# Performance work log

Measured on AMD Instinct MI355X. Metric: run time of the kernel, lower is better.

## Reference

```python
import jax, jax.numpy as jnp
import numpy as np

N_NODES = 10000
N_EDGES = 160000
C = 128           # channel multiplicity
D_DOWN = 64       # node_feats_down '64x0e'
D_RAD = 8         # radial basis size
AVG_NEIGH = 16.0
INV_SQRT3 = 1.0 / np.sqrt(3.0)  # CG coeff for 1o x 1o -> 0e


def setup_inputs() -> dict:
    key = jax.random.key(0)
    ks = jax.random.split(key, 20)
    inp = {
        "node_attrs": jax.random.normal(ks[0], (N_NODES, 10), jnp.float32),
        "node_feats": jax.random.normal(ks[1], (N_NODES, 4 * C), jnp.float32),
        "edge_attrs": jax.random.normal(ks[2], (N_EDGES, 4), jnp.float32),
        "edge_feats": jax.random.uniform(ks[3], (N_EDGES, D_RAD), jnp.float32),
        "edge_index": jax.random.randint(ks[4], (N_EDGES, 2), 0, N_NODES, jnp.int32),
        # linear_up: 128x0e+128x1o -> 128x0e+128x1o (per-irrep channel mixing)
        "W_up0": jax.random.normal(ks[5], (C, C), jnp.float32),
        "W_up1": jax.random.normal(ks[6], (C, C), jnp.float32),
        # linear_down: 128x0e+128x1o -> 64x0e (only scalars map)
        "W_down": jax.random.normal(ks[7], (C, D_DOWN), jnp.float32),
        # radial MLP [136, 256, 256, 256, 512]
        "Wm0": jax.random.normal(ks[8], (D_RAD + 2 * D_DOWN, 256), jnp.float32),
        "Wm1": jax.random.normal(ks[9], (256, 256), jnp.float32),
        "Wm2": jax.random.normal(ks[10], (256, 256), jnp.float32),
        "Wm3": jax.random.normal(ks[11], (256, 4 * C), jnp.float32),
        # linear: irreps_mid (2x128x0e + 2x128x1o) -> 128x0e+128x1o
        "W_lin0": jax.random.normal(ks[12], (2 * C, C), jnp.float32),
        "W_lin1": jax.random.normal(ks[13], (2 * C, C), jnp.float32),
        # skip_linear: 128x0e+128x1o -> 128x0e+128x1o
        "W_skip0": jax.random.normal(ks[14], (C, C), jnp.float32),
        "W_skip1": jax.random.normal(ks[15], (C, C), jnp.float32),
    }
    return inp


def _split(x):
    # [N, 512] -> scalars [N,128], vectors [N,128,3]
    return x[:, :C], x[:, C:].reshape(-1, C, 3)


def _irrep_linear(s, v, W0, W1):
    # e3nn Linear with 1/sqrt(fan_in) normalization, per-irrep
    a = (s @ W0) / np.sqrt(C)
    b = jnp.einsum("nic,ij->njc", v, W1) / np.sqrt(C)
    return a, b


def reference(node_attrs, node_feats, edge_attrs, edge_feats, edge_index,
              W_up0, W_up1, W_down, Wm0, Wm1, Wm2, Wm3,
              W_lin0, W_lin1, W_skip0, W_skip1):
    n_nodes = node_feats.shape[0]
    sender = edge_index[:, 0]
    receiver = edge_index[:, 1]

    s, v = _split(node_feats)

    # skip connection
    sc_s, sc_v = _irrep_linear(s, v, W_skip0, W_skip1)
    sc = jnp.concatenate([sc_s, sc_v.reshape(n_nodes, 3 * C)], axis=-1)

    # linear_up / linear_down
    up_s, up_v = _irrep_linear(s, v, W_up0, W_up1)
    down = (s @ W_down) / np.sqrt(C)  # [N, 64]

    # radial MLP on augmented edge feats
    aug = jnp.concatenate([edge_feats, down[sender], down[receiver]], axis=-1)  # [E,136]
    h = jax.nn.silu((aug @ Wm0) / np.sqrt(aug.shape[-1]))
    h = jax.nn.silu((h @ Wm1) / np.sqrt(256.0))
    h = jax.nn.silu((h @ Wm2) / np.sqrt(256.0))
    tpw = (h @ Wm3) / np.sqrt(256.0)  # [E, 512]
    w1, w2, w3, w4 = tpw[:, :C], tpw[:, C:2*C], tpw[:, 2*C:3*C], tpw[:, 3*C:]

    # per-edge CG tensor product (uvu, external weights)
    xs = up_s[sender]           # [E,128] gathered 0e
    xv = up_v[sender]           # [E,128,3] gathered 1o
    y0 = edge_attrs[:, :1]      # [E,1]   sh 0e
    yv = edge_attrs[:, 1:4]     # [E,3]   sh 1o

    out0a = w1 * xs * y0                                       # 0e x 0e -> 0e
    out0b = w4 * jnp.einsum("eic,ec->ei", xv, yv) * INV_SQRT3  # 1o x 1o -> 0e
    out1a = (w2 * xs)[:, :, None] * yv[:, None, :]             # 0e x 1o -> 1o
    out1b = w3[:, :, None] * xv * y0[:, :, None]               # 1o x 0e -> 1o

    mid0 = jnp.concatenate([out0a, out0b], axis=-1)  # [E,256]
    mid1 = jnp.concatenate([out1a, out1b], axis=1)   # [E,256,3]

    # scatter-sum messages to receivers
    m0 = jax.ops.segment_sum(mid0, receiver, num_segments=n_nodes)
    m1 = jax.ops.segment_sum(mid1, receiver, num_segments=n_nodes)

    # final per-irrep linear, divided by avg_num_neighbors
    msg_s = (m0 @ W_lin0) / np.sqrt(2.0 * C) / AVG_NEIGH                       # [N,128]
    msg_v = jnp.einsum("nic,ij->njc", m1, W_lin1) / np.sqrt(2.0 * C) / AVG_NEIGH  # [N,128,3]

    # reshape_irreps: [N, channels, 1+3]
    out = jnp.concatenate([msg_s[:, :, None], msg_v], axis=-1)  # [N,128,4]
    return out, sc
```

## Files before the change

### kernel.cpp

```cpp
#include <hip/hip_runtime.h>
#include <cmath>

#define NN 10000
#define NE 160000
#define INV_SQRT_C 0.08838834764831845f
#define INV_SQRT3F 0.5773502691896258f

typedef _Float16 f16x8 __attribute__((ext_vector_type(8)));
typedef _Float16 f16x4 __attribute__((ext_vector_type(4)));
typedef _Float16 f16x2 __attribute__((ext_vector_type(2)));
typedef float    f32x4 __attribute__((ext_vector_type(4)));

__device__ __forceinline__ float silu_f(float x) {
  return x / (1.f + __expf(-x));
}

__device__ __forceinline__ void wconv_one(
    int bx, const float* __restrict__ src, _Float16* __restrict__ dst,
    int Korig, int Kpad, int N, float scale, int P) {
  int total = Kpad * N;
  for (int t = bx * 256 + threadIdx.x; t < total; t += 128 * 256) {
    int n = t % N;
    int k = t / N;
    int kb = k >> 5, kk = k & 31;
    int sub = n & (P - 1);
    int n_l = (n & ~(P - 1)) | ((sub & 15) * (P >> 4) + (sub >> 4));
    float v = (k < Korig) ? src[(size_t)k * N + n_l] * scale : 0.f;
    dst[((size_t)(kb * N + n) << 5) + kk] = (_Float16)v;
  }
}

__global__ __launch_bounds__(256) void prep(
    const float* __restrict__ s0, const float* __restrict__ s1,
    const float* __restrict__ s2, const float* __restrict__ s3,
    const float* __restrict__ s4, const float* __restrict__ s5,
    _Float16* __restrict__ d0, _Float16* __restrict__ d1,
    _Float16* __restrict__ d2, _Float16* __restrict__ d3,
    _Float16* __restrict__ d4, _Float16* __restrict__ d5,
    const float* __restrict__ feats,
    const float* __restrict__ W_up0, const float* __restrict__ W_skip0,
    const float* __restrict__ W_down,
    const float* __restrict__ W_up1, const float* __restrict__ W_skip1,
    _Float16* __restrict__ UPH, _Float16* __restrict__ DOWNH,
    float* __restrict__ out_sc,
    const int* __restrict__ edge_index,
    int* __restrict__ CNT, int* __restrict__ CNT2) {
  __shared__ float ls[16 * 512];
  const int b = blockIdx.x;
  const int t = threadIdx.x;

  if (b < 768) {
    const int job = b >> 7, bx = b & 127;
    switch (job) {
      case 0: wconv_one(bx, s0, d0, 136, 160, 256, 0.08574929257125442f, 64); break;
      case 1: wconv_one(bx, s1, d1, 256, 256, 256, 0.0625f, 64); break;
      case 2: wconv_one(bx, s2, d2, 256, 256, 256, 0.0625f, 64); break;
      case 3: wconv_one(bx, s3, d3, 256, 256, 512, 0.0625f, 32); break;
      case 4: wconv_one(bx, s4, d4, 256, 256, 128, 1.0f / 256.0f, 32); break;
      default: wconv_one(bx, s5, d5, 256, 256, 128, 1.0f / 256.0f, 32); break;
    }
    return;
  }
  if (b >= 2018) {
    int e = (b - 2018) * 256 + t;
    if (e < NE) {
      int2 sr = *(const int2*)&edge_index[(size_t)e * 2];
      atomicAdd(&CNT[sr.y], 1);
      atomicAdd(&CNT2[sr.x], 1);
    }
    return;
  }

  const int nb = b - 768;
  if (nb < 625) {
    const int n0 = nb * 16;
    for (int f = t; f < 16 * 128; f += 256) {
      int r = f >> 7, c = f & 127;
      ls[r * 128 + c] = feats[(size_t)(n0 + r) * 512 + c];
    }
    __syncthreads();
    {
      int j = t & 127, g = t >> 7;
      float au[8] = {0, 0, 0, 0, 0, 0, 0, 0};
      float ak[8] = {0, 0, 0, 0, 0, 0, 0, 0};
      for (int i = 0; i < 128; ++i) {
        float wu = W_up0[(size_t)i * 128 + j];
        float wk = W_skip0[(size_t)i * 128 + j];
#pragma unroll
        for (int r = 0; r < 8; ++r) {
          float s = ls[(g * 8 + r) * 128 + i];
          au[r] += s * wu;
          ak[r] += s * wk;
        }
      }
#pragma unroll
      for (int r = 0; r < 8; ++r) {
        int n = n0 + g * 8 + r;
        UPH[(size_t)n * 512 + j] = (_Float16)(au[r] * INV_SQRT_C);
        out_sc[(size_t)n * 512 + j] = ak[r] * INV_SQRT_C;
      }
    }
    {
      int j = t & 63, g = t >> 6;
      float ad[4] = {0, 0, 0, 0};
      for (int i = 0; i < 128; ++i) {
        float wd = W_down[(size_t)i * 64 + j];
#pragma unroll
        for (int r = 0; r < 4; ++r) ad[r] += ls[(g * 4 + r) * 128 + i] * wd;
      }
#pragma unroll
      for (int r = 0; r < 4; ++r)
        DOWNH[(size_t)(n0 + g * 4 + r) * 64 + j] = (_Float16)(ad[r] * INV_SQRT_C);
    }
  } else {
    const int n0 = (nb - 625) * 16;
    for (int f = t; f < 16 * 384; f += 256) {
      int r = f / 384, c = f % 384;
      int i = c / 3, cc = c - i * 3;
      ls[(r * 128 + i) * 4 + cc] = feats[(size_t)(n0 + r) * 512 + 128 + c];
    }
    __syncthreads();
    const float4* lv = (const float4*)ls;
    int j = t & 127, g = t >> 7;
    float au[8][3], ak[8][3];
#pragma unroll
    for (int r = 0; r < 8; ++r)
#pragma unroll
      for (int c = 0; c < 3; ++c) { au[r][c] = 0.f; ak[r][c] = 0.f; }
    for (int i = 0; i < 128; ++i) {
      float wu = W_up1[(size_t)i * 128 + j];
      float wk = W_skip1[(size_t)i * 128 + j];
#pragma unroll
      for (int r = 0; r < 8; ++r) {
        float4 v = lv[(g * 8 + r) * 128 + i];
        au[r][0] += v.x * wu; au[r][1] += v.y * wu; au[r][2] += v.z * wu;
        ak[r][0] += v.x * wk; ak[r][1] += v.y * wk; ak[r][2] += v.z * wk;
      }
    }
#pragma unroll
    for (int r = 0; r < 8; ++r) {
      int n = n0 + g * 8 + r;
#pragma unroll
      for (int c = 0; c < 3; ++c) {
        UPH[(size_t)n * 512 + 128 + j * 3 + c] = (_Float16)(au[r][c] * INV_SQRT_C);
        out_sc[(size_t)n * 512 + 128 + j * 3 + c] = ak[r][c] * INV_SQRT_C;
      }
    }
  }
}

__device__ __forceinline__ void scan_one(const int* __restrict__ CNT,
                                         int* __restrict__ OFF,
                                         int* __restrict__ CUR, int* ts) {
  const int t = threadIdx.x;
  const int base = t * 10;
  int loc[10];
  int s = 0;
#pragma unroll
  for (int i = 0; i < 10; ++i) {
    int idx = base + i;
    int v = (idx < NN) ? CNT[idx] : 0;
    loc[i] = s;
    s += v;
  }
  ts[t] = s;
  __syncthreads();
  for (int off = 1; off < 1024; off <<= 1) {
    int v = (t >= off) ? ts[t - off] : 0;
    __syncthreads();
    ts[t] += v;
    __syncthreads();
  }
  int tp = (t > 0) ? ts[t - 1] : 0;
#pragma unroll
  for (int i = 0; i < 10; ++i) {
    int idx = base + i;
    if (idx < NN) {
      OFF[idx] = tp + loc[i];
      CUR[idx] = tp + loc[i];
    }
  }
  if (t == 1023) OFF[NN] = ts[1023];
}

__global__ __launch_bounds__(1024) void k_scan2(
    const int* __restrict__ CNT, int* __restrict__ OFF, int* __restrict__ CUR,
    const int* __restrict__ CNT2, int* __restrict__ OFF2, int* __restrict__ CUR2) {
  __shared__ int ts[1024];
  if (blockIdx.x == 0) scan_one(CNT, OFF, CUR, ts);
  else                 scan_one(CNT2, OFF2, CUR2, ts);
}

__global__ void k_fill2(const int* __restrict__ edge_index,
                        int* __restrict__ CUR, int* __restrict__ EIDX,
                        int* __restrict__ CUR2, int* __restrict__ SIDX) {
  int e = blockIdx.x * blockDim.x + threadIdx.x;
  if (e < NE) {
    int2 sr = *(const int2*)&edge_index[(size_t)e * 2];
    int ps = atomicAdd(&CUR2[sr.x], 1);
    SIDX[ps] = e;
    int pr = atomicAdd(&CUR[sr.y], 1);
    EIDX[pr] = ps;
  }
}

__device__ __forceinline__ void mlp_layer_256(
    const _Float16* In, _Float16* Out, const _Float16* __restrict__ Wz,
    int m, int g, int wv) {
  f32x4 acc[4][4];
  f32x4 zero4 = {0.f, 0.f, 0.f, 0.f};
#pragma unroll
  for (int rt = 0; rt < 4; ++rt)
#pragma unroll
    for (int ct = 0; ct < 4; ++ct) acc[rt][ct] = zero4;

#pragma unroll
  for (int kb = 0; kb < 8; ++kb) {
    f16x8 a[4], b[4];
#pragma unroll
    for (int rt = 0; rt < 4; ++rt) {
      int row = rt * 16 + m;
      a[rt] = *(const f16x8*)&In[row * 256 + (((kb * 2 + (g >> 1)) ^ m) << 4) + (g & 1) * 8];
    }
#pragma unroll
    for (int ct = 0; ct < 4; ++ct)
      b[ct] = *(const f16x8*)&Wz[((size_t)(kb * 256 + wv * 64 + ct * 16 + m) << 5) + g * 8];
#pragma unroll
    for (int rt = 0; rt < 4; ++rt)
#pragma unroll
      for (int ct = 0; ct < 4; ++ct)
        acc[rt][ct] = __builtin_amdgcn_mfma_f32_16x16x32_f16(a[rt], b[ct], acc[rt][ct], 0, 0, 0);
  }
#pragma unroll
  for (int rt = 0; rt < 4; ++rt)
#pragma unroll
    for (int q = 0; q < 4; ++q) {
      int row = rt * 16 + g * 4 + q;
      f16x4 pk;
#pragma unroll
      for (int ct = 0; ct < 4; ++ct) pk[ct] = (_Float16)silu_f(acc[rt][ct][q]);
      int blk = (wv * 4 + (m >> 2)) ^ (row & 15);
      *(f16x4*)&Out[row * 256 + (blk << 4) + (m & 3) * 4] = pk;
    }
}

__global__ __launch_bounds__(256, 2) void edge_mlp(
    const float* __restrict__ edge_attrs,
    const float* __restrict__ edge_feats,
    const int* __restrict__ edge_index,
    const int* __restrict__ SIDX,
    const _Float16* __restrict__ DOWNH,
    const _Float16* __restrict__ UPH,
    const _Float16* __restrict__ W0h, const _Float16* __restrict__ W1h,
    const _Float16* __restrict__ W2h, const _Float16* __restrict__ W3h,
    const _Float16* __restrict__ WL0h, const _Float16* __restrict__ WL1h,
    _Float16* __restrict__ MIDs) {
  __shared__ _Float16 HA[64 * 256];
  __shared__ _Float16 HB[64 * 256];

  const int tid = threadIdx.x;
  const int lane = tid & 63;
  const int wv = tid >> 6;
  const int m = lane & 15;
  const int g = lane >> 4;
  const int e0 = blockIdx.x * 64;
  const int nw = wv * 64;

  int el_r[4], snd_r[4], rcv_r[4];
#pragma unroll
  for (int rt = 0; rt < 4; ++rt) {
    el_r[rt] = SIDX[e0 + rt * 16 + m];
    int2 sr = *(const int2*)&edge_index[(size_t)el_r[rt] * 2];
    snd_r[rt] = sr.x;
    rcv_r[rt] = sr.y;
  }

  f32x4 zero4 = {0.f, 0.f, 0.f, 0.f};
  f16x8 zf = {0, 0, 0, 0, 0, 0, 0, 0};

  {
    f32x4 acc[4][4];
#pragma unroll
    for (int rt = 0; rt < 4; ++rt)
#pragma unroll
      for (int ct = 0; ct < 4; ++ct) acc[rt][ct] = zero4;

#pragma unroll
    for (int kb = 0; kb < 5; ++kb) {
      const int k0 = kb * 32 + g * 8;
      f16x8 a[4], b[4];
#pragma unroll
      for (int rt = 0; rt < 4; ++rt) {
        if (k0 == 0) {
          const float* ef = &edge_feats[(size_t)el_r[rt] * 8];
          float4 f0 = *(const float4*)ef;
          float4 f1 = *(const float4*)(ef + 4);
          f16x8 av;
          av[0] = (_Float16)f0.x; av[1] = (_Float16)f0.y;
          av[2] = (_Float16)f0.z; av[3] = (_Float16)f0.w;
          av[4] = (_Float16)f1.x; av[5] = (_Float16)f1.y;
          av[6] = (_Float16)f1.z; av[7] = (_Float16)f1.w;
          a[rt] = av;
        } else if (k0 < 72) {
          a[rt] = *(const f16x8*)&DOWNH[(size_t)snd_r[rt] * 64 + (k0 - 8)];
        } else if (k0 < 136) {
          a[rt] = *(const f16x8*)&DOWNH[(size_t)rcv_r[rt] * 64 + (k0 - 72)];
        } else {
          a[rt] = zf;
        }
      }
#pragma unroll
      for (int ct = 0; ct < 4; ++ct)
        b[ct] = *(const f16x8*)&W0h[((size_t)(kb * 256 + nw + ct * 16 + m) << 5) + g * 8];
#pragma unroll
      for (int rt = 0; rt < 4; ++rt)
#pragma unroll
        for (int ct = 0; ct < 4; ++ct)
          acc[rt][ct] = __builtin_amdgcn_mfma_f32_16x16x32_f16(a[rt], b[ct], acc[rt][ct], 0, 0, 0);
    }
#pragma unroll
    for (int rt = 0; rt < 4; ++rt)
#pragma unroll
      for (int q = 0; q < 4; ++q) {
        int row = rt * 16 + g * 4 + q;
        f16x4 pk;
#pragma unroll
        for (int ct = 0; ct < 4; ++ct) pk[ct] = (_Float16)silu_f(acc[rt][ct][q]);
        int blk = (wv * 4 + (m >> 2)) ^ (row & 15);
        *(f16x4*)&HA[row * 256 + (blk << 4) + (m & 3) * 4] = pk;
      }
  }
  __syncthreads();

  mlp_layer_256(HA, HB, W1h, m, g, wv);
  __syncthreads();
  mlp_layer_256(HB, HA, W2h, m, g, wv);
  __syncthreads();

  _Float16* SW = HB;
  _Float16* SP = HB + 64 * 128;

  const int e_loc = lane;
  const int ers = (e_loc ^ (e_loc >> 3)) & 7;
  const int elc = SIDX[e0 + e_loc];
  const int snd_e = edge_index[(size_t)elc * 2];
  const _Float16* uprow = &UPH[(size_t)snd_e * 512];

  auto qgemm = [&](int qbase, f32x4 (&accq)[4][2]) {
#pragma unroll
    for (int rt = 0; rt < 4; ++rt)
#pragma unroll
      for (int ct = 0; ct < 2; ++ct) accq[rt][ct] = zero4;
#pragma unroll
    for (int kb = 0; kb < 8; ++kb) {
      f16x8 a[4], b[2];
#pragma unroll
      for (int rt = 0; rt < 4; ++rt) {
        int row = rt * 16 + m;
        a[rt] = *(const f16x8*)&HA[row * 256 + (((kb * 2 + (g >> 1)) ^ m) << 4) + (g & 1) * 8];
      }
#pragma unroll
      for (int ct = 0; ct < 2; ++ct)
        b[ct] = *(const f16x8*)&W3h[((size_t)(kb * 512 + qbase + wv * 32 + ct * 16 + m) << 5) + g * 8];
#pragma unroll
      for (int rt = 0; rt < 4; ++rt)
#pragma unroll
        for (int ct = 0; ct < 2; ++ct)
          accq[rt][ct] = __builtin_amdgcn_mfma_f32_16x16x32_f16(a[rt], b[ct], accq[rt][ct], 0, 0, 0);
    }
  };

  auto sw_write = [&](const f32x4 (&accq)[4][2]) {
#pragma unroll
    for (int rt = 0; rt < 4; ++rt)
#pragma unroll
      for (int r4 = 0; r4 < 4; ++r4) {
        int row = rt * 16 + g * 4 + r4;
        int rs = (row ^ (row >> 3)) & 7;
        f16x2 pk;
        pk[0] = (_Float16)accq[rt][0][r4];
        pk[1] = (_Float16)accq[rt][1][r4];
        int blk = ((wv * 2 + (m >> 3)) ^ rs) & 7;
        *(f16x2*)&SW[row * 128 + (blk << 4) + (m & 7) * 2] = pk;
      }
  };

  auto fold = [&](const _Float16* __restrict__ WLh, int qpart, f32x4 (&P)[4][2]) {
#pragma unroll
    for (int rt = 0; rt < 4; ++rt)
#pragma unroll
      for (int ct = 0; ct < 2; ++ct) P[rt][ct] = zero4;
#pragma unroll
    for (int kb = 0; kb < 4; ++kb) {
      f16x8 a[4], b[2];
#pragma unroll
      for (int rt = 0; rt < 4; ++rt) {
        int row = rt * 16 + m;
        int rs = (row ^ (row >> 3)) & 7;
        a[rt] = *(const f16x8*)&SP[row * 128 + ((((kb * 2 + (g >> 1)) ^ rs) & 7) << 4) + (g & 1) * 8];
      }
#pragma unroll
      for (int ct = 0; ct < 2; ++ct)
        b[ct] = *(const f16x8*)&WLh[((size_t)((qpart * 4 + kb) * 128 + wv * 32 + ct * 16 + m) << 5) + g * 8];
#pragma unroll
      for (int rt = 0; rt < 4; ++rt)
#pragma unroll
        for (int ct = 0; ct < 2; ++ct)
          P[rt][ct] = __builtin_amdgcn_mfma_f32_16x16x32_f16(a[rt], b[ct], P[rt][ct], 0, 0, 0);
    }
  };

  auto tp_xs = [&]() {
#pragma unroll
    for (int cch = 0; cch < 4; ++cch) {
      int ib = nw / 2 + cch * 8;
      int blk = ((ib >> 4) ^ ers) & 7;
      int off = e_loc * 128 + (blk << 4) + (ib & 15);
      f16x8 swv = *(const f16x8*)&SW[off];
      f16x8 upv = *(const f16x8*)&uprow[ib];
      f16x8 pr = swv * upv;
      *(f16x8*)&SP[off] = pr;
    }
  };

  _Float16 xvb[96];
  auto load_xv = [&]() {
#pragma unroll
    for (int u = 0; u < 12; ++u) {
      f16x8 t = *(const f16x8*)&uprow[128 + wv * 96 + u * 8];
#pragma unroll
      for (int z = 0; z < 8; ++z) xvb[u * 8 + z] = t[z];
    }
  };

  auto tp_w4 = [&]() {
    float4 ea = *(const float4*)&edge_attrs[(size_t)elc * 4];
#pragma unroll
    for (int cch = 0; cch < 4; ++cch) {
      int ib = nw / 2 + cch * 8;
      int blk = ((ib >> 4) ^ ers) & 7;
      int off = e_loc * 128 + (blk << 4) + (ib & 15);
      f16x8 swv = *(const f16x8*)&SW[off];
      f16x8 outv;
#pragma unroll
      for (int z = 0; z < 8; ++z) {
        int k = cch * 8 + z;
        float d = (float)xvb[k * 3] * ea.y + (float)xvb[k * 3 + 1] * ea.z +
                  (float)xvb[k * 3 + 2] * ea.w;
        outv[z] = (_Float16)((float)swv[z] * d);
      }
      *(f16x8*)&SP[off] = outv;
    }
  };

  auto tp_w3 = [&](int c) {
#pragma unroll
    for (int cch = 0; cch < 4; ++cch) {
      int ib = nw / 2 + cch * 8;
      int blk = ((ib >> 4) ^ ers) & 7;
      int off = e_loc * 128 + (blk << 4) + (ib & 15);
      f16x8 swv = *(const f16x8*)&SW[off];
      f16x8 outv;
#pragma unroll
      for (int z = 0; z < 8; ++z) {
        int k = cch * 8 + z;
        outv[z] = swv[z] * xvb[k * 3 + c];
      }
      *(f16x8*)&SP[off] = outv;
    }
  };

  f32x4 accqA[4][2], accqB[4][2];
  f32x4 P1[4][2], P4[4][2], P2[4][2], P3[4][2];

  qgemm(0, accqA);
  sw_write(accqA);
  tp_xs();
  qgemm(384, accqB);
  __syncthreads();
  fold(WL0h, 0, P1);
  sw_write(accqB);
  load_xv();
  __syncthreads();
  tp_w4();
  qgemm(128, accqA);
  __syncthreads();
  fold(WL0h, 1, P4);
  sw_write(accqA);

#pragma unroll
  for (int rt = 0; rt < 4; ++rt)
#pragma unroll
    for (int r4 = 0; r4 < 4; ++r4) {
      int row = rt * 16 + g * 4 + r4;
      int elw = SIDX[e0 + row];
      float4 ea = *(const float4*)&edge_attrs[(size_t)elw * 4];
      f16x2 pk;
      pk[0] = (_Float16)(ea.x * P1[rt][0][r4] + INV_SQRT3F * P4[rt][0][r4]);
      pk[1] = (_Float16)(ea.x * P1[rt][1][r4] + INV_SQRT3F * P4[rt][1][r4]);
      *(f16x2*)&MIDs[(size_t)(e0 + row) * 512 + wv * 32 + m * 2] = pk;
    }
  __syncthreads();
  tp_xs();
  qgemm(256, accqB);
  __syncthreads();
  fold(WL1h, 0, P2);
  sw_write(accqB);
  __syncthreads();

#pragma unroll
  for (int c = 0; c < 3; ++c) {
    tp_w3(c);
    __syncthreads();
    fold(WL1h, 1, P3);
#pragma unroll
    for (int rt = 0; rt < 4; ++rt)
#pragma unroll
      for (int r4 = 0; r4 < 4; ++r4) {
        int row = rt * 16 + g * 4 + r4;
        int elw = SIDX[e0 + row];
        float4 ea = *(const float4*)&edge_attrs[(size_t)elw * 4];
        float yvc = (c == 0) ? ea.y : (c == 1) ? ea.z : ea.w;
        f16x2 pk;
        pk[0] = (_Float16)(yvc * P2[rt][0][r4] + ea.x * P3[rt][0][r4]);
        pk[1] = (_Float16)(yvc * P2[rt][1][r4] + ea.x * P3[rt][1][r4]);
        *(f16x2*)&MIDs[(size_t)(e0 + row) * 512 + 128 + c * 128 + wv * 32 + m * 2] = pk;
      }
    if (c < 2) __syncthreads();
  }
}

__global__ __launch_bounds__(256) void gather_msg(
    const _Float16* __restrict__ MIDs, const int* __restrict__ OFF,
    const int* __restrict__ EIDX, float* __restrict__ out) {
  __shared__ int eb[256];
  __shared__ float os[512];
  const int n = blockIdx.x;
  const int t = threadIdx.x;
  const int beg = OFF[n], end = OFF[n + 1];
  float a0 = 0.f, a1 = 0.f;
  for (int base = beg; base < end; base += 256) {
    int cnt = min(256, end - base);
    __syncthreads();
    if (t < cnt) eb[t] = EIDX[base + t];
    __syncthreads();
    int k = 0;
    for (; k + 4 <= cnt; k += 4) {
      int e0_ = eb[k], e1_ = eb[k + 1], e2_ = eb[k + 2], e3_ = eb[k + 3];
      f16x2 v0 = *(const f16x2*)&MIDs[(size_t)e0_ * 512 + t * 2];
      f16x2 v1 = *(const f16x2*)&MIDs[(size_t)e1_ * 512 + t * 2];
      f16x2 v2 = *(const f16x2*)&MIDs[(size_t)e2_ * 512 + t * 2];
      f16x2 v3 = *(const f16x2*)&MIDs[(size_t)e3_ * 512 + t * 2];
      a0 += (float)v0[0] + (float)v1[0] + (float)v2[0] + (float)v3[0];
      a1 += (float)v0[1] + (float)v1[1] + (float)v2[1] + (float)v3[1];
    }
    for (; k < cnt; ++k) {
      f16x2 v = *(const f16x2*)&MIDs[(size_t)eb[k] * 512 + t * 2];
      a0 += (float)v[0];
      a1 += (float)v[1];
    }
  }
#pragma unroll
  for (int u = 0; u < 2; ++u) {
    int x = t * 2 + u;
    float a = u ? a1 : a0;
    int dst;
    if (x < 128) {
      dst = x * 4;
    } else {
      int xm = x - 128;
      int c = xm >> 7, j = xm & 127;
      dst = j * 4 + 1 + c;
    }
    os[dst] = a;
  }
  __syncthreads();
  *(float2*)&out[(size_t)n * 512 + t * 2] = *(const float2*)&os[t * 2];
}

extern "C" void kernel_launch(void* const* d_in, const int* in_sizes, int n_in,
                              void* d_out, int out_size, void* d_ws, size_t ws_size,
                              hipStream_t stream) {
  const float* node_feats = (const float*)d_in[1];
  const float* edge_attrs = (const float*)d_in[2];
  const float* edge_feats = (const float*)d_in[3];
  const int*   edge_index = (const int*)d_in[4];
  const float* W_up0   = (const float*)d_in[5];
  const float* W_up1   = (const float*)d_in[6];
  const float* W_down  = (const float*)d_in[7];
  const float* Wm0     = (const float*)d_in[8];
  const float* Wm1     = (const float*)d_in[9];
  const float* Wm2     = (const float*)d_in[10];
  const float* Wm3     = (const float*)d_in[11];
  const float* W_lin0  = (const float*)d_in[12];
  const float* W_lin1  = (const float*)d_in[13];
  const float* W_skip0 = (const float*)d_in[14];
  const float* W_skip1 = (const float*)d_in[15];
  float* out = (float*)d_out;

  char* ws = (char*)d_ws;
  size_t off = 0;
  auto alloc = [&](size_t bytes) {
    void* p = ws + off;
    off = (off + bytes + 255) & ~(size_t)255;
    return p;
  };
  _Float16* UPH   = (_Float16*)alloc((size_t)NN * 512 * 2);
  _Float16* DOWNH = (_Float16*)alloc((size_t)NN * 64 * 2);
  _Float16* W0h   = (_Float16*)alloc(160 * 256 * 2);
  _Float16* W1h   = (_Float16*)alloc(256 * 256 * 2);
  _Float16* W2h   = (_Float16*)alloc(256 * 256 * 2);
  _Float16* W3h   = (_Float16*)alloc(256 * 512 * 2);
  _Float16* WL0h  = (_Float16*)alloc(256 * 128 * 2);
  _Float16* WL1h  = (_Float16*)alloc(256 * 128 * 2);
  int*      CNTS  = (int*)alloc((size_t)2 * NN * 4);
  int*      CNT   = CNTS;
  int*      CNT2  = CNTS + NN;
  int*      OFF   = (int*)alloc((size_t)(NN + 1) * 4);
  int*      CUR   = (int*)alloc((size_t)NN * 4);
  int*      EIDX  = (int*)alloc((size_t)NE * 4);
  int*      OFF2  = (int*)alloc((size_t)(NN + 1) * 4);
  int*      CUR2  = (int*)alloc((size_t)NN * 4);
  int*      SIDX  = (int*)alloc((size_t)NE * 4);
  _Float16* MIDs  = (_Float16*)alloc((size_t)NE * 512 * 2);

  hipMemsetAsync(CNTS, 0, (size_t)2 * NN * 4, stream);

  prep<<<2643, 256, 0, stream>>>(Wm0, Wm1, Wm2, Wm3, W_lin0, W_lin1,
                                 W0h, W1h, W2h, W3h, WL0h, WL1h,
                                 node_feats, W_up0, W_skip0, W_down,
                                 W_up1, W_skip1,
                                 UPH, DOWNH, out + (size_t)NN * 512,
                                 edge_index, CNT, CNT2);

  k_scan2<<<2, 1024, 0, stream>>>(CNT, OFF, CUR, CNT2, OFF2, CUR2);
  k_fill2<<<625, 256, 0, stream>>>(edge_index, CUR, EIDX, CUR2, SIDX);

  edge_mlp<<<2500, 256, 0, stream>>>(edge_attrs, edge_feats, edge_index, SIDX,
                                     DOWNH, UPH, W0h, W1h, W2h, W3h, WL0h, WL1h,
                                     MIDs);
  gather_msg<<<NN, 256, 0, stream>>>(MIDs, OFF, EIDX, out);
}
```

Before: 461.5 us.

## Move node up/skip/down linears to MFMA fp16 GEMM kernel

Splits the old prep kernel into a weight-conversion/edge-count kernel and a new prep2 kernel. prep2 computes the up, skip and down node linears with fp16 MFMA tiles from swizzled shared memory instead of scalar fp32 FMA loops. Up and skip weights are packed into one fp16 buffer so both outputs share the A tiles. It adds an extra kernel launch and computes the fp32 skip output from fp16-rounded inputs, which costs accuracy.

```diff
diff --git a/kernel.cpp b/kernel.cpp
--- a/kernel.cpp
+++ b/kernel.cpp
@@ -30,25 +30,46 @@
   }
 }
 
-__global__ __launch_bounds__(256) void prep(
+__device__ __forceinline__ void wconv_pair(
+    int bx, const float* __restrict__ A, const float* __restrict__ B,
+    _Float16* __restrict__ dst, float scale) {
+  int tgl = bx * 256 + threadIdx.x;
+  int n = tgl & 255;
+  int k = tgl >> 8;
+  int kb = k >> 5, kk = k & 31;
+  int sub = n & 63;
+  int n_l = (n & ~63) | ((sub & 15) * 4 + (sub >> 4));
+  float v = ((n_l < 128) ? A[(size_t)k * 128 + n_l]
+                         : B[(size_t)k * 128 + (n_l - 128)]) * scale;
+  dst[((size_t)(kb * 256 + n) << 5) + kk] = (_Float16)v;
+}
+
+__device__ __forceinline__ void wconv_dn(
+    int bx, const float* __restrict__ src, _Float16* __restrict__ dst,
+    float scale) {
+  int tgl = bx * 256 + threadIdx.x;
+  int n = tgl & 63;
+  int k = tgl >> 6;
+  int kb = k >> 5, kk = k & 31;
+  float v = src[(size_t)k * 64 + n] * scale;
+  dst[((size_t)(kb * 64 + n) << 5) + kk] = (_Float16)v;
+}
+
+__global__ __launch_bounds__(256) void wconv9(
     const float* __restrict__ s0, const float* __restrict__ s1,
     const float* __restrict__ s2, const float* __restrict__ s3,
     const float* __restrict__ s4, const float* __restrict__ s5,
     _Float16* __restrict__ d0, _Float16* __restrict__ d1,
     _Float16* __restrict__ d2, _Float16* __restrict__ d3,
     _Float16* __restrict__ d4, _Float16* __restrict__ d5,
-    const float* __restrict__ feats,
     const float* __restrict__ W_up0, const float* __restrict__ W_skip0,
+    const float* __restrict__ W_up1, const float* __restrict__ W_skip1,
     const float* __restrict__ W_down,
-    const float* __restrict__ W_up1, const float* __restrict__ W_skip1,
-    _Float16* __restrict__ UPH, _Float16* __restrict__ DOWNH,
-    float* __restrict__ out_sc,
+    _Float16* __restrict__ WS0h, _Float16* __restrict__ WS1h,
+    _Float16* __restrict__ WDh,
     const int* __restrict__ edge_index,
     int* __restrict__ CNT, int* __restrict__ CNT2) {
-  __shared__ float ls[16 * 512];
   const int b = blockIdx.x;
-  const int t = threadIdx.x;
-
   if (b < 768) {
     const int job = b >> 7, bx = b & 127;
     switch (job) {
@@ -59,93 +80,167 @@
       case 4: wconv_one(bx, s4, d4, 256, 256, 128, 1.0f / 256.0f, 32); break;
       default: wconv_one(bx, s5, d5, 256, 256, 128, 1.0f / 256.0f, 32); break;
     }
-    return;
-  }
-  if (b >= 2018) {
-    int e = (b - 2018) * 256 + t;
+  } else if (b < 896) {
+    wconv_pair(b - 768, W_up0, W_skip0, WS0h, INV_SQRT_C);
+  } else if (b < 1024) {
+    wconv_pair(b - 896, W_up1, W_skip1, WS1h, INV_SQRT_C);
+  } else if (b < 1056) {
+    wconv_dn(b - 1024, W_down, WDh, INV_SQRT_C);
+  } else {
+    int e = (b - 1056) * 256 + threadIdx.x;
     if (e < NE) {
       int2 sr = *(const int2*)&edge_index[(size_t)e * 2];
       atomicAdd(&CNT[sr.y], 1);
       atomicAdd(&CNT2[sr.x], 1);
     }
-    return;
-  }
-
-  const int nb = b - 768;
-  if (nb < 625) {
-    const int n0 = nb * 16;
-    for (int f = t; f < 16 * 128; f += 256) {
-      int r = f >> 7, c = f & 127;
-      ls[r * 128 + c] = feats[(size_t)(n0 + r) * 512 + c];
+  }
+}
+
+__global__ __launch_bounds__(256) void prep2(
+    const float* __restrict__ feats,
+    const _Float16* __restrict__ WS0h, const _Float16* __restrict__ WS1h,
+    const _Float16* __restrict__ WDh,
+    _Float16* __restrict__ UPH, _Float16* __restrict__ DOWNH,
+    float* __restrict__ out_sc) {
+  __shared__ _Float16 As[64 * 128];
+  const int b = blockIdx.x;
+  const int t = threadIdx.x;
+  const int lane = t & 63;
+  const int wv = t >> 6;
+  const int m = lane & 15;
+  const int g = lane >> 4;
+  f32x4 zero4 = {0.f, 0.f, 0.f, 0.f};
+  f16x8 zf = {0, 0, 0, 0, 0, 0, 0, 0};
+
+  if (b < 157) {
+    const int n0 = b * 64;
+    for (int idx = t; idx < 1024; idx += 256) {
+      int r = idx >> 4, c8 = idx & 15;
+      int n = n0 + r;
+      f16x8 av = zf;
+      if (n < NN) {
+        const float* src = &feats[(size_t)n * 512 + c8 * 8];
+        float4 f0 = *(const float4*)src;
+        float4 f1 = *(const float4*)(src + 4);
+        av[0] = (_Float16)f0.x; av[1] = (_Float16)f0.y;
+        av[2] = (_Float16)f0.z; av[3] = (_Float16)f0.w;
+        av[4] = (_Float16)f1.x; av[5] = (_Float16)f1.y;
+        av[6] = (_Float16)f1.z; av[7] = (_Float16)f1.w;
+      }
+      int sb = (c8 >> 1) ^ (r & 7);
+      *(f16x8*)&As[r * 128 + (sb << 4) + (c8 & 1) * 8] = av;
     }
     __syncthreads();
-    {
-      int j = t & 127, g = t >> 7;
-      float au[8] = {0, 0, 0, 0, 0, 0, 0, 0};
-      float ak[8] = {0, 0, 0, 0, 0, 0, 0, 0};
-      for (int i = 0; i < 128; ++i) {
-        float wu = W_up0[(size_t)i * 128 + j];
-        float wk = W_skip0[(size_t)i * 128 + j];
-#pragma unroll
-        for (int r = 0; r < 8; ++r) {
-          float s = ls[(g * 8 + r) * 128 + i];
-          au[r] += s * wu;
-          ak[r] += s * wk;
+
+    f32x4 acc[4][4];
+    f32x4 acc2[4];
+#pragma unroll
+    for (int rt = 0; rt < 4; ++rt) {
+      acc2[rt] = zero4;
+#pragma unroll
+      for (int ct = 0; ct < 4; ++ct) acc[rt][ct] = zero4;
+    }
+#pragma unroll
+    for (int kb = 0; kb < 4; ++kb) {
+      f16x8 a[4], bf[4];
+#pragma unroll
+      for (int rt = 0; rt < 4; ++rt) {
+        int row = rt * 16 + m;
+        a[rt] = *(const f16x8*)&As[row * 128 +
+                 ((((kb * 2 + (g >> 1)) ^ (m & 7)) & 7) << 4) + (g & 1) * 8];
+      }
+#pragma unroll
+      for (int ct = 0; ct < 4; ++ct)
+        bf[ct] = *(const f16x8*)&WS0h[((size_t)(kb * 256 + wv * 64 + ct * 16 + m) << 5) + g * 8];
+      f16x8 bd = *(const f16x8*)&WDh[((size_t)(kb * 64 + wv * 16 + m) << 5) + g * 8];
+#pragma unroll
+      for (int rt = 0; rt < 4; ++rt) {
+#pragma unroll
+        for (int ct = 0; ct < 4; ++ct)
+          acc[rt][ct] = __builtin_amdgcn_mfma_f32_16x16x32_f16(a[rt], bf[ct], acc[rt][ct], 0, 0, 0);
+        acc2[rt] = __builtin_amdgcn_mfma_f32_16x16x32_f16(a[rt], bd, acc2[rt], 0, 0, 0);
+      }
+    }
+#pragma unroll
+    for (int rt = 0; rt < 4; ++rt)
+#pragma unroll
+      for (int q = 0; q < 4; ++q) {
+        int row = rt * 16 + g * 4 + q;
+        int n = n0 + row;
+        if (n >= NN) continue;
+        if (wv < 2) {
+          f16x4 pk;
+#pragma unroll
+          for (int ct = 0; ct < 4; ++ct) pk[ct] = (_Float16)acc[rt][ct][q];
+          *(f16x4*)&UPH[(size_t)n * 512 + wv * 64 + m * 4] = pk;
+        } else {
+          float4 p4 = {acc[rt][0][q], acc[rt][1][q], acc[rt][2][q], acc[rt][3][q]};
+          *(float4*)&out_sc[(size_t)n * 512 + (wv - 2) * 64 + m * 4] = p4;
         }
-      }
-#pragma unroll
-      for (int r = 0; r < 8; ++r) {
-        int n = n0 + g * 8 + r;
-        UPH[(size_t)n * 512 + j] = (_Float16)(au[r] * INV_SQRT_C);
-        out_sc[(size_t)n * 512 + j] = ak[r] * INV_SQRT_C;
-      }
-    }
-    {
-      int j = t & 63, g = t >> 6;
-      float ad[4] = {0, 0, 0, 0};
-      for (int i = 0; i < 128; ++i) {
-        float wd = W_down[(size_t)i * 64 + j];
-#pragma unroll
-        for (int r = 0; r < 4; ++r) ad[r] += ls[(g * 4 + r) * 128 + i] * wd;
-      }
-#pragma unroll
-      for (int r = 0; r < 4; ++r)
-        DOWNH[(size_t)(n0 + g * 4 + r) * 64 + j] = (_Float16)(ad[r] * INV_SQRT_C);
-    }
-  } else {
-    const int n0 = (nb - 625) * 16;
-    for (int f = t; f < 16 * 384; f += 256) {
-      int r = f / 384, c = f % 384;
-      int i = c / 3, cc = c - i * 3;
-      ls[(r * 128 + i) * 4 + cc] = feats[(size_t)(n0 + r) * 512 + 128 + c];
+        DOWNH[(size_t)n * 64 + wv * 16 + m] = (_Float16)acc2[rt][q];
+      }
+  } else if (b < 626) {
+    const int v0 = (b - 157) * 64;
+    for (int idx = t; idx < 1024; idx += 256) {
+      int r = idx >> 4, c8 = idx & 15;
+      int rg = v0 + r;
+      f16x8 av = zf;
+      if (rg < 3 * NN) {
+        int n = rg / 3, c = rg - n * 3;
+        const float* src = &feats[(size_t)n * 512 + 128 + c];
+#pragma unroll
+        for (int z = 0; z < 8; ++z) av[z] = (_Float16)src[(c8 * 8 + z) * 3];
+      }
+      int sb = (c8 >> 1) ^ (r & 7);
+      *(f16x8*)&As[r * 128 + (sb << 4) + (c8 & 1) * 8] = av;
     }
     __syncthreads();
-    const float4* lv = (const float4*)ls;
-    int j = t & 127, g = t >> 7;
-    float au[8][3], ak[8][3];
-#pragma unroll
-    for (int r = 0; r < 8; ++r)
-#pragma unroll
-      for (int c = 0; c < 3; ++c) { au[r][c] = 0.f; ak[r][c] = 0.f; }
-    for (int i = 0; i < 128; ++i) {
-      float wu = W_up1[(size_t)i * 128 + j];
-      float wk = W_skip1[(size_t)i * 128 + j];
-#pragma unroll
-      for (int r = 0; r < 8; ++r) {
-        float4 v = lv[(g * 8 + r) * 128 + i];
-        au[r][0] += v.x * wu; au[r][1] += v.y * wu; au[r][2] += v.z * wu;
-        ak[r][0] += v.x * wk; ak[r][1] += v.y * wk; ak[r][2] += v.z * wk;
-      }
-    }
-#pragma unroll
-    for (int r = 0; r < 8; ++r) {
-      int n = n0 + g * 8 + r;
-#pragma unroll
-      for (int c = 0; c < 3; ++c) {
-        UPH[(size_t)n * 512 + 128 + j * 3 + c] = (_Float16)(au[r][c] * INV_SQRT_C);
-        out_sc[(size_t)n * 512 + 128 + j * 3 + c] = ak[r][c] * INV_SQRT_C;
-      }
-    }
+
+    f32x4 acc[4][4];
+#pragma unroll
+    for (int rt = 0; rt < 4; ++rt)
+#pragma unroll
+      for (int ct = 0; ct < 4; ++ct) acc[rt][ct] = zero4;
+#pragma unroll
+    for (int kb = 0; kb < 4; ++kb) {
+      f16x8 a[4], bf[4];
+#pragma unroll
+      for (int rt = 0; rt < 4; ++rt) {
+        int row = rt * 16 + m;
+        a[rt] = *(const f16x8*)&As[row * 128 +
+                 ((((kb * 2 + (g >> 1)) ^ (m & 7)) & 7) << 4) + (g & 1) * 8];
+      }
+#pragma unroll
+      for (int ct = 0; ct < 4; ++ct)
+        bf[ct] = *(const f16x8*)&WS1h[((size_t)(kb * 256 + wv * 64 + ct * 16 + m) << 5) + g * 8];
+#pragma unroll
+      for (int rt = 0; rt < 4; ++rt)
+#pragma unroll
+        for (int ct = 0; ct < 4; ++ct)
+          acc[rt][ct] = __builtin_amdgcn_mfma_f32_16x16x32_f16(a[rt], bf[ct], acc[rt][ct], 0, 0, 0);
+    }
+#pragma unroll
+    for (int rt = 0; rt < 4; ++rt)
+#pragma unroll
+      for (int q = 0; q < 4; ++q) {
+        int row = rt * 16 + g * 4 + q;
+        int rg = v0 + row;
+        if (rg >= 3 * NN) continue;
+        int n = rg / 3, c = rg - (rg / 3) * 3;
+        if (wv < 2) {
+#pragma unroll
+          for (int ct = 0; ct < 4; ++ct) {
+            int j = wv * 64 + m * 4 + ct;
+            UPH[(size_t)n * 512 + 128 + j * 3 + c] = (_Float16)acc[rt][ct][q];
+          }
+        } else {
+#pragma unroll
+          for (int ct = 0; ct < 4; ++ct) {
+            int j = (wv - 2) * 64 + m * 4 + ct;
+            out_sc[(size_t)n * 512 + 128 + j * 3 + c] = acc[rt][ct][q];
+          }
+        }
+      }
   }
 }
 
@@ -613,6 +708,9 @@
   _Float16* W3h   = (_Float16*)alloc(256 * 512 * 2);
   _Float16* WL0h  = (_Float16*)alloc(256 * 128 * 2);
   _Float16* WL1h  = (_Float16*)alloc(256 * 128 * 2);
+  _Float16* WS0h  = (_Float16*)alloc(128 * 256 * 2);
+  _Float16* WS1h  = (_Float16*)alloc(128 * 256 * 2);
+  _Float16* WDh   = (_Float16*)alloc(128 * 64 * 2);
   int*      CNTS  = (int*)alloc((size_t)2 * NN * 4);
   int*      CNT   = CNTS;
   int*      CNT2  = CNTS + NN;
@@ -626,12 +724,14 @@
 
   hipMemsetAsync(CNTS, 0, (size_t)2 * NN * 4, stream);
 
-  prep<<<2643, 256, 0, stream>>>(Wm0, Wm1, Wm2, Wm3, W_lin0, W_lin1,
-                                 W0h, W1h, W2h, W3h, WL0h, WL1h,
-                                 node_feats, W_up0, W_skip0, W_down,
-                                 W_up1, W_skip1,
-                                 UPH, DOWNH, out + (size_t)NN * 512,
-                                 edge_index, CNT, CNT2);
+  wconv9<<<1681, 256, 0, stream>>>(Wm0, Wm1, Wm2, Wm3, W_lin0, W_lin1,
+                                   W0h, W1h, W2h, W3h, WL0h, WL1h,
+                                   W_up0, W_skip0, W_up1, W_skip1, W_down,
+                                   WS0h, WS1h, WDh,
+                                   edge_index, CNT, CNT2);
+
+  prep2<<<626, 256, 0, stream>>>(node_feats, WS0h, WS1h, WDh,
+                                 UPH, DOWNH, out + (size_t)NN * 512);
 
   k_scan2<<<2, 1024, 0, stream>>>(CNT, OFF, CUR, CNT2, OFF2, CUR2);
   k_fill2<<<625, 256, 0, stream>>>(edge_index, CUR, EIDX, CUR2, SIDX);
```

New measurement: 457.7 us. Within noise of the previous version (-0.8%).
